# Kernel tuning notes

Measured on AMD Instinct MI355X. Metric: run time of the kernel, lower is better.

Reference implementation:

```python
import jax, jax.numpy as jnp
import numpy as np

N_NODES = 50000
N_EDGES = 800000
C_FEAT = 96
HID = 96
C_CONST = 0.005


def _psi(v):
    return jnp.sign(v) * jnp.log(jnp.abs(v) + 1.0)


def setup_inputs() -> dict:
    key = jax.random.key(0)
    ks = jax.random.split(key, 16)
    d_e_in = 2 * C_FEAT + 2
    d_h_in = 2 * C_FEAT
    def w(k, fan_in, fan_out):
        return jax.random.normal(k, (fan_in, fan_out), jnp.float32) * (1.0 / np.sqrt(fan_in))
    return {
        "x": jax.random.normal(ks[0], (N_NODES, 4), jnp.float32),
        "h": jax.random.normal(ks[1], (N_NODES, C_FEAT), jnp.float32),
        "edge_i": jax.random.randint(ks[2], (N_EDGES,), 0, N_NODES, jnp.int32),
        "edge_j": jax.random.randint(ks[3], (N_EDGES,), 0, N_NODES, jnp.int32),
        "We1": w(ks[4], d_e_in, HID), "be1": jnp.zeros((HID,), jnp.float32),
        "We2": w(ks[5], HID, HID), "be2": jnp.zeros((HID,), jnp.float32),
        "Wm": w(ks[6], HID, 1), "bm": jnp.zeros((1,), jnp.float32),
        "Wh1": w(ks[7], d_h_in, HID), "bh1": jnp.zeros((HID,), jnp.float32),
        "Wh2": w(ks[8], HID, C_FEAT), "bh2": jnp.zeros((C_FEAT,), jnp.float32),
        "Wx1": w(ks[9], HID, HID), "bx1": jnp.zeros((HID,), jnp.float32),
        "Wx2": w(ks[10], HID, 1),  # bias-free last phi_x layer
    }


def reference(x, h, edge_i, edge_j, We1, be1, We2, be2, Wm, bm,
              Wh1, bh1, Wh2, bh2, Wx1, bx1, Wx2):
    n = x.shape[0]
    x_i = x[edge_i]            # (K,4)
    x_j = x[edge_j]            # (K,4)
    # Minkowski invariants: 2*t-component - full Euclidean sum == (+,-,-,-)
    d2 = jnp.square(x_i - x_j)
    norms = 2.0 * d2[..., 0] - jnp.sum(d2, axis=-1)
    z = x_i * x_j
    prods = 2.0 * z[..., 0] - jnp.sum(z, axis=-1)
    norms = _psi(norms)[:, None]   # (K,1)
    prods = _psi(prods)[:, None]   # (K,1)

    e_in = jnp.concatenate([h[edge_i], h[edge_j], norms, prods], axis=-1)  # (K,2C+2)
    m = jax.nn.relu(jax.nn.relu(e_in @ We1 + be1) @ We2 + be2)             # (K,HID)
    w_gate = jax.nn.sigmoid(m @ Wm + bm)                                   # (K,1)

    wm = jax.ops.segment_sum(w_gate * m, edge_i, num_segments=n)          # (N,HID)
    dh = jax.nn.relu(jnp.concatenate([h, wm], axis=-1) @ Wh1 + bh1) @ Wh2 + bh2
    h_out = h + dh

    phi_x = jax.nn.relu(m @ Wx1 + bx1) @ Wx2                              # (K,1)
    vals = phi_x * x_j                                                     # (K,4)
    s = jax.ops.segment_sum(vals, edge_i, num_segments=n)                 # (N,4)
    cnt = jax.ops.segment_sum(jnp.ones((vals.shape[0],), vals.dtype), edge_i, num_segments=n)
    mean = jnp.where(cnt[:, None] > 0, s / jnp.maximum(cnt[:, None], 1.0), 0.0)
    x_out = x + C_CONST * mean
    return (h_out, x_out)
```

## Files before the change

### kernel.cpp

```cpp
#include <hip/hip_runtime.h>
#include <math.h>

#define NN 50000
#define NE 800000
#define NB 196

typedef __attribute__((ext_vector_type(8))) short short8v;
typedef __attribute__((ext_vector_type(4))) float f32x4;

__device__ __forceinline__ int rfl(int v) { return __builtin_amdgcn_readfirstlane(v); }
__device__ __forceinline__ unsigned short f2bf(float f) {
  unsigned u = __float_as_uint(f);
  u += 0x7FFFu + ((u >> 16) & 1u);
  return (unsigned short)(u >> 16);
}
__device__ __forceinline__ unsigned pk2(float a, float b) {
  return (unsigned)f2bf(a) | ((unsigned)f2bf(b) << 16);
}
__device__ __forceinline__ float bflo(unsigned u) { return __uint_as_float(u << 16); }
__device__ __forceinline__ float bfhi(unsigned u) { return __uint_as_float(u & 0xFFFF0000u); }

__global__ void khist(const int* __restrict__ ei, int* __restrict__ cnt) {
  const int i = blockIdx.x * 256 + threadIdx.x;
  atomicAdd(&cnt[ei[i]], 1);
}

__global__ void kscanA(const int* __restrict__ cnt, int* __restrict__ pre,
                       int* __restrict__ bsum) {
  __shared__ int ps[256];
  const int b = blockIdx.x, t = threadIdx.x, idx = b * 256 + t;
  const int v = (idx < NN) ? cnt[idx] : 0;
  ps[t] = v;
  __syncthreads();
  for (int off = 1; off < 256; off <<= 1) {
    const int u = (t >= off) ? ps[t - off] : 0;
    __syncthreads();
    ps[t] += u;
    __syncthreads();
  }
  if (idx < NN) pre[idx] = ps[t] - v;
  if (t == 255) bsum[b] = ps[255];
}

__global__ void kscanB(const int* __restrict__ bsum, int* __restrict__ boff) {
  __shared__ int ps[256];
  const int t = threadIdx.x;
  const int v = (t < NB) ? bsum[t] : 0;
  ps[t] = v;
  __syncthreads();
  for (int off = 1; off < 256; off <<= 1) {
    const int u = (t >= off) ? ps[t - off] : 0;
    __syncthreads();
    ps[t] += u;
    __syncthreads();
  }
  if (t < NB) boff[t] = ps[t] - v;
}

__global__ void kscanC(const int* __restrict__ pre, const int* __restrict__ boff,
                       int* __restrict__ base, int* __restrict__ cursor) {
  const int b = blockIdx.x, t = threadIdx.x, idx = b * 256 + t;
  if (idx < NN) {
    const int v = pre[idx] + boff[b];
    base[idx] = v;
    cursor[idx] = v;
  }
  if (idx == 0) base[NN] = NE;
}

__global__ void kperm(const int* __restrict__ ei, const int* __restrict__ ej,
                      int* __restrict__ cursor,
                      int* __restrict__ eis, int* __restrict__ ejs) {
  const int i = blockIdx.x * 256 + threadIdx.x;
  const int vi = ei[i];
  const int pos = atomicAdd(&cursor[vi], 1);
  eis[pos] = vi;
  ejs[pos] = ej[i];
}

__global__ void kwprep(const float* __restrict__ We1, const float* __restrict__ We2,
                       const float* __restrict__ Wx1, const float* __restrict__ Wh1,
                       const float* __restrict__ Wh2,
                       unsigned short* __restrict__ We1p, unsigned short* __restrict__ We2p,
                       unsigned short* __restrict__ Wx1p, unsigned short* __restrict__ Wh1p,
                       unsigned short* __restrict__ Wh2p) {
  const int t = blockIdx.x * 256 + threadIdx.x;
  const int j = t & 7, lane = (t >> 3) & 63;
  const int kk = (lane >> 4) * 8 + j;
  const int nn = lane & 15;
  {
    const int tile = t >> 9, tk = tile / 12, tn = tile % 12;
    const int k = tk * 32 + kk, n2 = tn * 16 + nn;
    const float v = (n2 < 96) ? We1[k * 96 + n2] : We1[(96 + k) * 96 + (n2 - 96)];
    We1p[t] = f2bf(v);
  }
  {
    const int tile = t >> 9, tk = tile / 6, tn = tile % 6;
    const int k = tk * 32 + kk, n = tn * 16 + nn;
    Wh1p[t] = f2bf(Wh1[k * 96 + n]);
  }
  if (t < 9216) {
    const int tile = t >> 9, tk = tile / 6, tn = tile % 6;
    const int k = tk * 32 + kk, n = tn * 16 + nn;
    We2p[t] = f2bf(We2[k * 96 + n]);
    Wx1p[t] = f2bf(Wx1[k * 96 + n]);
    Wh2p[t] = f2bf(Wh2[k * 96 + n]);
  }
}

__global__ __launch_bounds__(256, 4) void k0_AB(const float* __restrict__ h,
                                                const unsigned short* __restrict__ We1p,
                                                unsigned short* __restrict__ Abf,
                                                unsigned short* __restrict__ Bbf) {
  __shared__ __align__(16) unsigned short hbT[64 * 104];
  __shared__ __align__(16) unsigned short outT[64 * 200];
  const int tid = threadIdx.x;
  const int nb = blockIdx.x * 64;
  {
    const int e = tid & 63, q = tid >> 6;
    const int node = nb + e;
    const int nc = node < NN ? node : NN - 1;
    const float* hr = h + (long)nc * 96 + q * 24;
    unsigned* dst = (unsigned*)hbT + e * 52 + q * 12;
    #pragma unroll
    for (int c = 0; c < 6; ++c) {
      const float4 v = *(const float4*)(hr + c * 4);
      dst[c * 2]     = pk2(v.x, v.y);
      dst[c * 2 + 1] = pk2(v.z, v.w);
    }
  }
  __syncthreads();
  const int l = tid & 63, w = tid >> 6, cg = l & 15, rg = l >> 4;
  {
    const short8v* Wp = (const short8v*)We1p;
    const unsigned short* ar = hbT + (w * 16 + cg) * 104;
    const short8v af0 = *(const short8v*)(ar + rg * 8);
    const short8v af1 = *(const short8v*)(ar + 32 + rg * 8);
    const short8v af2 = *(const short8v*)(ar + 64 + rg * 8);
    #pragma unroll
    for (int tn = 0; tn < 12; ++tn) {
      f32x4 acc = (f32x4){0.f, 0.f, 0.f, 0.f};
      acc = __builtin_amdgcn_mfma_f32_16x16x32_bf16(af0, Wp[(0 * 12 + tn) * 64 + l], acc, 0, 0, 0);
      acc = __builtin_amdgcn_mfma_f32_16x16x32_bf16(af1, Wp[(1 * 12 + tn) * 64 + l], acc, 0, 0, 0);
      acc = __builtin_amdgcn_mfma_f32_16x16x32_bf16(af2, Wp[(2 * 12 + tn) * 64 + l], acc, 0, 0, 0);
      #pragma unroll
      for (int r = 0; r < 4; ++r)
        outT[(w * 16 + rg * 4 + r) * 200 + tn * 16 + cg] = f2bf(acc[r]);
    }
  }
  __syncthreads();
  {
    const int e = tid & 63, q = tid >> 6;
    const int node = nb + e;
    if (node < NN) {
      const unsigned* src = (const unsigned*)outT + e * 100;
      if (q < 2) {
        uint4* dA = (uint4*)(Abf + (size_t)node * 96);
        #pragma unroll
        for (int i = 0; i < 6; ++i) dA[q * 6 + i] = *(const uint4*)(src + (q * 6 + i) * 4);
      } else {
        uint4* dB = (uint4*)(Bbf + (size_t)node * 96);
        #pragma unroll
        for (int i = 0; i < 6; ++i) dB[(q - 2) * 6 + i] = *(const uint4*)(src + 48 + ((q - 2) * 6 + i) * 4);
      }
    }
  }
}

__global__ __launch_bounds__(256, 8) void k1_edge(const float* __restrict__ x,
    const unsigned short* __restrict__ Abf, const unsigned short* __restrict__ Bbf,
    const int* __restrict__ eis, const int* __restrict__ ejs,
    const float* __restrict__ We1, const float* __restrict__ be1,
    const unsigned short* __restrict__ We2p, const float* __restrict__ be2,
    const float* __restrict__ Wm, const float* __restrict__ bm,
    const unsigned short* __restrict__ Wx1p, const float* __restrict__ bx1,
    const float* __restrict__ Wx2,
    float* __restrict__ wmo, float* __restrict__ svo) {
  __shared__ __align__(16) unsigned short actT[64 * 104];
  __shared__ float gl[64];
  __shared__ float phil[64];
  __shared__ float xjl[64 * 4];
  __shared__ int vseq[66];

  const int tid = threadIdx.x;
  const float bm0 = bm[0];
  const int tb = blockIdx.x * 64;

  {
    const int e2 = tid & 63, fb = (tid >> 6) * 24;
    const int vi = eis[tb + e2], vj = ejs[tb + e2];
    const float4 xi = *(const float4*)(x + (long)vi * 4);
    const float4 xj = *(const float4*)(x + (long)vj * 4);
    if (tid < 64) {
      vseq[1 + e2] = vi;
      xjl[e2 * 4 + 0] = xj.x; xjl[e2 * 4 + 1] = xj.y;
      xjl[e2 * 4 + 2] = xj.z; xjl[e2 * 4 + 3] = xj.w;
    }
    if (tid == 0) {
      vseq[0]  = (tb > 0) ? eis[tb - 1] : -1;
      vseq[65] = (tb + 64 < NE) ? eis[tb + 64] : -1;
    }
    const float d0 = xi.x - xj.x, d1 = xi.y - xj.y, d2 = xi.z - xj.z, d3 = xi.w - xj.w;
    const float nrm = d0 * d0 - d1 * d1 - d2 * d2 - d3 * d3;
    const float prd = xi.x * xj.x - xi.y * xj.y - xi.z * xj.z - xi.w * xj.w;
    const float pn = copysignf(logf(fabsf(nrm) + 1.f), nrm);
    const float pp = copysignf(logf(fabsf(prd) + 1.f), prd);
    const uint4* Ar = (const uint4*)(Abf + (size_t)vi * 96 + fb);
    const uint4* Br = (const uint4*)(Bbf + (size_t)vj * 96 + fb);
    const uint4 A0 = Ar[0], A1 = Ar[1], A2 = Ar[2];
    const uint4 B0 = Br[0], B1 = Br[1], B2 = Br[2];
    unsigned ua[12], ub[12];
    ua[0]=A0.x; ua[1]=A0.y; ua[2]=A0.z; ua[3]=A0.w; ua[4]=A1.x; ua[5]=A1.y;
    ua[6]=A1.z; ua[7]=A1.w; ua[8]=A2.x; ua[9]=A2.y; ua[10]=A2.z; ua[11]=A2.w;
    ub[0]=B0.x; ub[1]=B0.y; ub[2]=B0.z; ub[3]=B0.w; ub[4]=B1.x; ub[5]=B1.y;
    ub[6]=B1.z; ub[7]=B1.w; ub[8]=B2.x; ub[9]=B2.y; ub[10]=B2.z; ub[11]=B2.w;
    unsigned* arow = (unsigned*)actT + e2 * 52 + fb / 2;
    #pragma unroll
    for (int p = 0; p < 12; ++p) {
      const int f = fb + 2 * p;
      const float lo = fmaxf(bflo(ua[p]) + bflo(ub[p]) + pn * We1[192 * 96 + f] + pp * We1[193 * 96 + f] + be1[f], 0.f);
      const float hi = fmaxf(bfhi(ua[p]) + bfhi(ub[p]) + pn * We1[192 * 96 + f + 1] + pp * We1[193 * 96 + f + 1] + be1[f + 1], 0.f);
      arow[p] = pk2(lo, hi);
    }
  }
  __syncthreads();

  const int l = tid & 63, w = tid >> 6;
  const int cg = l & 15, rg = l >> 4;
  const short8v* Wp2 = (const short8v*)We2p;
  const short8v* Wpx = (const short8v*)Wx1p;

  {
    const unsigned short* ar = actT + (w * 16 + cg) * 104;
    const short8v af0 = *(const short8v*)(ar + rg * 8);
    const short8v af1 = *(const short8v*)(ar + 32 + rg * 8);
    const short8v af2 = *(const short8v*)(ar + 64 + rg * 8);
    f32x4 acc[6];
    #pragma unroll
    for (int tn = 0; tn < 6; ++tn) acc[tn] = (f32x4){0.f, 0.f, 0.f, 0.f};
    #pragma unroll
    for (int tn = 0; tn < 6; ++tn) {
      acc[tn] = __builtin_amdgcn_mfma_f32_16x16x32_bf16(af0, Wp2[(0 * 6 + tn) * 64 + l], acc[tn], 0, 0, 0);
      acc[tn] = __builtin_amdgcn_mfma_f32_16x16x32_bf16(af1, Wp2[(1 * 6 + tn) * 64 + l], acc[tn], 0, 0, 0);
      acc[tn] = __builtin_amdgcn_mfma_f32_16x16x32_bf16(af2, Wp2[(2 * 6 + tn) * 64 + l], acc[tn], 0, 0, 0);
    }
    float gp[4] = {0.f, 0.f, 0.f, 0.f};
    #pragma unroll
    for (int tn = 0; tn < 6; ++tn) {
      const int col = tn * 16 + cg;
      const float b = be2[col], wmw = Wm[col];
      #pragma unroll
      for (int r = 0; r < 4; ++r) {
        const float v = fmaxf(acc[tn][r] + b, 0.f);
        gp[r] = fmaf(v, wmw, gp[r]);
        actT[(w * 16 + rg * 4 + r) * 104 + col] = (short)f2bf(v);
      }
    }
    #pragma unroll
    for (int r = 0; r < 4; ++r) {
      float s = gp[r];
      s += __shfl_xor(s, 1); s += __shfl_xor(s, 2);
      s += __shfl_xor(s, 4); s += __shfl_xor(s, 8);
      if (cg == 0) gl[w * 16 + rg * 4 + r] = 1.f / (1.f + expf(-(s + bm0)));
    }
  }
  __syncthreads();

  {
    const unsigned short* mr = actT + (w * 16 + cg) * 104;
    const short8v mf0 = *(const short8v*)(mr + rg * 8);
    const short8v mf1 = *(const short8v*)(mr + 32 + rg * 8);
    const short8v mf2 = *(const short8v*)(mr + 64 + rg * 8);
    f32x4 acc[6];
    #pragma unroll
    for (int tn = 0; tn < 6; ++tn) acc[tn] = (f32x4){0.f, 0.f, 0.f, 0.f};
    #pragma unroll
    for (int tn = 0; tn < 6; ++tn) {
      acc[tn] = __builtin_amdgcn_mfma_f32_16x16x32_bf16(mf0, Wpx[(0 * 6 + tn) * 64 + l], acc[tn], 0, 0, 0);
      acc[tn] = __builtin_amdgcn_mfma_f32_16x16x32_bf16(mf1, Wpx[(1 * 6 + tn) * 64 + l], acc[tn], 0, 0, 0);
      acc[tn] = __builtin_amdgcn_mfma_f32_16x16x32_bf16(mf2, Wpx[(2 * 6 + tn) * 64 + l], acc[tn], 0, 0, 0);
    }
    float pp2[4] = {0.f, 0.f, 0.f, 0.f};
    #pragma unroll
    for (int tn = 0; tn < 6; ++tn) {
      const int col = tn * 16 + cg;
      const float b = bx1[col], wxw = Wx2[col];
      #pragma unroll
      for (int r = 0; r < 4; ++r)
        pp2[r] = fmaf(fmaxf(acc[tn][r] + b, 0.f), wxw, pp2[r]);
    }
    #pragma unroll
    for (int r = 0; r < 4; ++r) {
      float s = pp2[r];
      s += __shfl_xor(s, 1); s += __shfl_xor(s, 2);
      s += __shfl_xor(s, 4); s += __shfl_xor(s, 8);
      if (cg == 0) phil[w * 16 + rg * 4 + r] = s;
    }
  }
  __syncthreads();

  if (tid < 200) {
    const bool isx = tid >= 192;
    const int col  = isx ? ((tid - 192) & 3) : (tid < 96 ? tid : tid - 96);
    const int half = isx ? ((tid - 192) >> 2) : (tid < 96 ? 0 : 1);
    const int s_lo = half * 32, s_hi = s_lo + 32;
    float acc = 0.f;
    bool clean = (vseq[s_lo] != vseq[s_lo + 1]);
    for (int e = s_lo; e < s_hi; ++e) {
      float val;
      if (isx) val = phil[e] * xjl[e * 4 + col];
      else     val = gl[e] * __uint_as_float(((unsigned)actT[e * 104 + col]) << 16);
      acc += val;
      const bool gend = (vseq[e + 1] != vseq[e + 2]);
      const bool last = (e == s_hi - 1);
      if (gend || last) {
        const int node = vseq[e + 1];
        float* dst = isx ? (svo + (size_t)node * 4 + col)
                         : (wmo + (size_t)node * 96 + col);
        if (clean && gend) *dst = acc; else atomicAdd(dst, acc);
        acc = 0.f; clean = true;
        if (last) break;
      }
    }
  }
}

__global__ __launch_bounds__(256, 4) void k3ab(const float* __restrict__ h,
    const float* __restrict__ wmv,
    const unsigned short* __restrict__ Wh1p, const float* __restrict__ bh1,
    const unsigned short* __restrict__ Wh2p, const float* __restrict__ bh2,
    const float* __restrict__ x, const float* __restrict__ svm,
    const int* __restrict__ basep,
    float* __restrict__ hout, float* __restrict__ xout) {
  __shared__ __align__(16) unsigned short inT[64 * 200];
  __shared__ __align__(16) unsigned short tmpT[64 * 104];
  const int tid = threadIdx.x;
  const int nb = blockIdx.x * 64;
  {
    const int e = tid & 63, q = tid >> 6;
    const int node = nb + e;
    const int nc = node < NN ? node : NN - 1;
    const float* hr = h + (long)nc * 96 + q * 24;
    const float* wr = wmv + (long)nc * 96 + q * 24;
    unsigned* dh = (unsigned*)inT + e * 100 + q * 12;
    unsigned* dw = (unsigned*)inT + e * 100 + 48 + q * 12;
    #pragma unroll
    for (int c = 0; c < 6; ++c) {
      const float4 v = *(const float4*)(hr + c * 4);
      dh[c * 2]     = pk2(v.x, v.y);
      dh[c * 2 + 1] = pk2(v.z, v.w);
      const float4 u = *(const float4*)(wr + c * 4);
      dw[c * 2]     = pk2(u.x, u.y);
      dw[c * 2 + 1] = pk2(u.z, u.w);
    }
  }
  __syncthreads();
  const int l = tid & 63, w = tid >> 6, cg = l & 15, rg = l >> 4;
  {
    const unsigned short* ar = inT + (w * 16 + cg) * 200;
    short8v af[6];
    #pragma unroll
    for (int tk = 0; tk < 6; ++tk) af[tk] = *(const short8v*)(ar + tk * 32 + rg * 8);
    const short8v* Wp = (const short8v*)Wh1p;
    #pragma unroll
    for (int tn = 0; tn < 6; ++tn) {
      f32x4 acc = (f32x4){0.f, 0.f, 0.f, 0.f};
      #pragma unroll
      for (int tk = 0; tk < 6; ++tk)
        acc = __builtin_amdgcn_mfma_f32_16x16x32_bf16(af[tk], Wp[(tk * 6 + tn) * 64 + l], acc, 0, 0, 0);
      const int col = tn * 16 + cg;
      const float b = bh1[col];
      #pragma unroll
      for (int r = 0; r < 4; ++r)
        tmpT[(w * 16 + rg * 4 + r) * 104 + col] = f2bf(fmaxf(acc[r] + b, 0.f));
    }
  }
  __syncthreads();
  {
    float* oT = (float*)inT;
    const unsigned short* mr = tmpT + (w * 16 + cg) * 104;
    const short8v mf0 = *(const short8v*)(mr + rg * 8);
    const short8v mf1 = *(const short8v*)(mr + 32 + rg * 8);
    const short8v mf2 = *(const short8v*)(mr + 64 + rg * 8);
    const short8v* Wp = (const short8v*)Wh2p;
    #pragma unroll
    for (int tn = 0; tn < 6; ++tn) {
      f32x4 acc = (f32x4){0.f, 0.f, 0.f, 0.f};
      acc = __builtin_amdgcn_mfma_f32_16x16x32_bf16(mf0, Wp[(0 * 6 + tn) * 64 + l], acc, 0, 0, 0);
      acc = __builtin_amdgcn_mfma_f32_16x16x32_bf16(mf1, Wp[(1 * 6 + tn) * 64 + l], acc, 0, 0, 0);
      acc = __builtin_amdgcn_mfma_f32_16x16x32_bf16(mf2, Wp[(2 * 6 + tn) * 64 + l], acc, 0, 0, 0);
      const int col = tn * 16 + cg;
      const float b = bh2[col];
      #pragma unroll
      for (int r = 0; r < 4; ++r)
        oT[(w * 16 + rg * 4 + r) * 100 + col] = acc[r] + b;
    }
  }
  __syncthreads();
  {
    const int e = tid & 63, q = tid >> 6;
    const int node = nb + e;
    if (node < NN) {
      const float* src = (const float*)inT + e * 100 + q * 24;
      const float* hr = h + (size_t)node * 96 + q * 24;
      float* dst = hout + (size_t)node * 96 + q * 24;
      #pragma unroll
      for (int c = 0; c < 6; ++c) {
        const float4 s = *(const float4*)(src + c * 4);
        const float4 hv = *(const float4*)(hr + c * 4);
        *(float4*)(dst + c * 4) = make_float4(hv.x + s.x, hv.y + s.y, hv.z + s.z, hv.w + s.w);
      }
    }
  }
  if (tid < 64) {
    const int node = nb + tid;
    if (node < NN) {
      const int cnt = basep[node + 1] - basep[node];
      const float inv = cnt > 0 ? 1.f / (float)cnt : 0.f;
      const float4 s4 = *(const float4*)(svm + (long)node * 4);
      const float4 xv = *(const float4*)(x + (long)node * 4);
      *(float4*)(xout + (long)node * 4) =
          make_float4(xv.x + 0.005f * s4.x * inv, xv.y + 0.005f * s4.y * inv,
                      xv.z + 0.005f * s4.z * inv, xv.w + 0.005f * s4.w * inv);
    }
  }
}

extern "C" void kernel_launch(void* const* d_in, const int* in_sizes, int n_in,
                              void* d_out, int out_size, void* d_ws, size_t ws_size,
                              hipStream_t stream) {
  const float* x   = (const float*)d_in[0];
  const float* h   = (const float*)d_in[1];
  const int*   ei  = (const int*)d_in[2];
  const int*   ej  = (const int*)d_in[3];
  const float* We1 = (const float*)d_in[4];
  const float* be1 = (const float*)d_in[5];
  const float* We2 = (const float*)d_in[6];
  const float* be2 = (const float*)d_in[7];
  const float* Wm  = (const float*)d_in[8];
  const float* bm  = (const float*)d_in[9];
  const float* Wh1 = (const float*)d_in[10];
  const float* bh1 = (const float*)d_in[11];
  const float* Wh2 = (const float*)d_in[12];
  const float* bh2 = (const float*)d_in[13];
  const float* Wx1 = (const float*)d_in[14];
  const float* bx1 = (const float*)d_in[15];
  const float* Wx2 = (const float*)d_in[16];

  char* w = (char*)d_ws;
  unsigned short* Abf  = (unsigned short*)w;
  unsigned short* Bbf  = (unsigned short*)(w + 9600000);
  float* WMv  = (float*)(w + 19200000);
  float* SvM  = (float*)(w + 38400000);
  int*   cnt  = (int*)(w + 39200000);
  int*   base = (int*)(w + 39400000);
  int*   curs = (int*)(w + 39600064);
  unsigned short* We2p = (unsigned short*)(w + 39800064);
  unsigned short* Wx1p = (unsigned short*)(w + 39818496);
  unsigned short* We1p = (unsigned short*)(w + 39836928);
  unsigned short* Wh1p = (unsigned short*)(w + 39873792);
  unsigned short* Wh2p = (unsigned short*)(w + 39910656);
  int*   eis  = (int*)(w + 39929088);
  int*   ejs  = (int*)(w + 43129088);
  int*   pre  = (int*)(w + 46329088);
  int*   bsum = (int*)(w + 46529088);
  int*   boff = (int*)(w + 46529872);

  float* hout = (float*)d_out;
  float* xout = hout + 4800000;

  hipMemsetAsync(cnt, 0, NN * sizeof(int), stream);
  hipMemsetAsync(WMv, 0, (size_t)(4800000 + 200000) * sizeof(float), stream);
  khist<<<NE / 256, 256, 0, stream>>>(ei, cnt);
  kscanA<<<NB, 256, 0, stream>>>(cnt, pre, bsum);
  kscanB<<<1, 256, 0, stream>>>(bsum, boff);
  kscanC<<<NB, 256, 0, stream>>>(pre, boff, base, curs);
  kperm<<<NE / 256, 256, 0, stream>>>(ei, ej, curs, eis, ejs);
  kwprep<<<72, 256, 0, stream>>>(We1, We2, Wx1, Wh1, Wh2, We1p, We2p, Wx1p, Wh1p, Wh2p);
  k0_AB<<<782, 256, 0, stream>>>(h, We1p, Abf, Bbf);
  k1_edge<<<NE / 64, 256, 0, stream>>>(x, Abf, Bbf, eis, ejs, We1, be1, We2p, be2,
                                       Wm, bm, Wx1p, bx1, Wx2, WMv, SvM);
  k3ab<<<782, 256, 0, stream>>>(h, WMv, Wh1p, bh1, Wh2p, bh2, x, SvM, base, hout, xout);
}
```

Measured before the change: 316.3 us.

## Process 128 edges per block with two MFMA row tiles sharing weight loads

The edge kernel now handles 128 edges per 256-thread block instead of 64. Each wave computes two 16-row tiles so every loaded weight fragment feeds two MFMAs, and one barrier between the two GEMMs is dropped because each wave only touches its own rows. Segment boundaries are precomputed once into ballot bitmasks, and the reduction is split across threads in two passes. In exchange it uses more registers and LDS (launch bounds drop to 5 blocks per CU) and produces half as many blocks, which may lower occupancy and latency hiding for the gathers.

```diff
diff --git a/kernel.cpp b/kernel.cpp
--- a/kernel.cpp
+++ b/kernel.cpp
@@ -4,6 +4,7 @@
 #define NN 50000
 #define NE 800000
 #define NB 196
+#define TE 128
 
 typedef __attribute__((ext_vector_type(8))) short short8v;
 typedef __attribute__((ext_vector_type(4))) float f32x4;
@@ -167,7 +168,7 @@
   }
 }
 
-__global__ __launch_bounds__(256, 8) void k1_edge(const float* __restrict__ x,
+__global__ __launch_bounds__(256, 5) void k1_edge(const float* __restrict__ x,
     const unsigned short* __restrict__ Abf, const unsigned short* __restrict__ Bbf,
     const int* __restrict__ eis, const int* __restrict__ ejs,
     const float* __restrict__ We1, const float* __restrict__ be1,
@@ -176,29 +177,30 @@
     const unsigned short* __restrict__ Wx1p, const float* __restrict__ bx1,
     const float* __restrict__ Wx2,
     float* __restrict__ wmo, float* __restrict__ svo) {
-  __shared__ __align__(16) unsigned short actT[64 * 104];
-  __shared__ float gl[64];
-  __shared__ float phil[64];
-  __shared__ float xjl[64 * 4];
-  __shared__ int vseq[66];
+  __shared__ __align__(16) unsigned short actT[TE * 104];
+  __shared__ float gl[TE];
+  __shared__ float phil[TE];
+  __shared__ __align__(16) float xjl[TE * 4];
+  __shared__ int vseq[TE + 2];
+  __shared__ unsigned long long bmask[2];
 
   const int tid = threadIdx.x;
   const float bm0 = bm[0];
-  const int tb = blockIdx.x * 64;
-
-  {
-    const int e2 = tid & 63, fb = (tid >> 6) * 24;
+  const int tb = blockIdx.x * TE;
+
+  {
+    const int e2 = tid & 127, hf = tid >> 7;
+    const int fb = hf * 48;
     const int vi = eis[tb + e2], vj = ejs[tb + e2];
     const float4 xi = *(const float4*)(x + (long)vi * 4);
     const float4 xj = *(const float4*)(x + (long)vj * 4);
-    if (tid < 64) {
+    if (hf == 0) {
       vseq[1 + e2] = vi;
-      xjl[e2 * 4 + 0] = xj.x; xjl[e2 * 4 + 1] = xj.y;
-      xjl[e2 * 4 + 2] = xj.z; xjl[e2 * 4 + 3] = xj.w;
+      *(float4*)(xjl + e2 * 4) = xj;
     }
     if (tid == 0) {
-      vseq[0]  = (tb > 0) ? eis[tb - 1] : -1;
-      vseq[65] = (tb + 64 < NE) ? eis[tb + 64] : -1;
+      vseq[0] = (tb > 0) ? eis[tb - 1] : -1;
+      vseq[TE + 1] = (tb + TE < NE) ? eis[tb + TE] : -1;
     }
     const float d0 = xi.x - xj.x, d1 = xi.y - xj.y, d2 = xi.z - xj.z, d3 = xi.w - xj.w;
     const float nrm = d0 * d0 - d1 * d1 - d2 * d2 - d3 * d3;
@@ -207,119 +209,165 @@
     const float pp = copysignf(logf(fabsf(prd) + 1.f), prd);
     const uint4* Ar = (const uint4*)(Abf + (size_t)vi * 96 + fb);
     const uint4* Br = (const uint4*)(Bbf + (size_t)vj * 96 + fb);
-    const uint4 A0 = Ar[0], A1 = Ar[1], A2 = Ar[2];
-    const uint4 B0 = Br[0], B1 = Br[1], B2 = Br[2];
-    unsigned ua[12], ub[12];
-    ua[0]=A0.x; ua[1]=A0.y; ua[2]=A0.z; ua[3]=A0.w; ua[4]=A1.x; ua[5]=A1.y;
-    ua[6]=A1.z; ua[7]=A1.w; ua[8]=A2.x; ua[9]=A2.y; ua[10]=A2.z; ua[11]=A2.w;
-    ub[0]=B0.x; ub[1]=B0.y; ub[2]=B0.z; ub[3]=B0.w; ub[4]=B1.x; ub[5]=B1.y;
-    ub[6]=B1.z; ub[7]=B1.w; ub[8]=B2.x; ub[9]=B2.y; ub[10]=B2.z; ub[11]=B2.w;
-    unsigned* arow = (unsigned*)actT + e2 * 52 + fb / 2;
-    #pragma unroll
-    for (int p = 0; p < 12; ++p) {
-      const int f = fb + 2 * p;
-      const float lo = fmaxf(bflo(ua[p]) + bflo(ub[p]) + pn * We1[192 * 96 + f] + pp * We1[193 * 96 + f] + be1[f], 0.f);
-      const float hi = fmaxf(bfhi(ua[p]) + bfhi(ub[p]) + pn * We1[192 * 96 + f + 1] + pp * We1[193 * 96 + f + 1] + be1[f + 1], 0.f);
-      arow[p] = pk2(lo, hi);
-    }
-  }
-  __syncthreads();
+    const float* wA = We1 + 192 * 96 + fb;
+    const float* wB = We1 + 193 * 96 + fb;
+    const float* bE = be1 + fb;
+    unsigned* arow = (unsigned*)actT + e2 * 52 + hf * 24;
+    #pragma unroll
+    for (int c = 0; c < 6; ++c) {
+      const uint4 A4 = Ar[c], B4 = Br[c];
+      const unsigned au[4] = {A4.x, A4.y, A4.z, A4.w};
+      const unsigned bu[4] = {B4.x, B4.y, B4.z, B4.w};
+      #pragma unroll
+      for (int k2 = 0; k2 < 4; ++k2) {
+        const int f = c * 8 + k2 * 2;
+        const float lo = fmaxf(bflo(au[k2]) + bflo(bu[k2]) + pn * wA[f] + pp * wB[f] + bE[f], 0.f);
+        const float hi = fmaxf(bfhi(au[k2]) + bfhi(bu[k2]) + pn * wA[f + 1] + pp * wB[f + 1] + bE[f + 1], 0.f);
+        arow[c * 4 + k2] = pk2(lo, hi);
+      }
+    }
+  }
+  __syncthreads();
+
+  if (tid < TE) {
+    const int pred = (vseq[1 + tid] != vseq[2 + tid]) ? 1 : 0;
+    const unsigned long long mk = __ballot(pred);
+    if ((tid & 63) == 0) bmask[tid >> 6] = mk;
+  }
 
   const int l = tid & 63, w = tid >> 6;
   const int cg = l & 15, rg = l >> 4;
+  const int r0 = w * 32;
   const short8v* Wp2 = (const short8v*)We2p;
   const short8v* Wpx = (const short8v*)Wx1p;
 
   {
-    const unsigned short* ar = actT + (w * 16 + cg) * 104;
-    const short8v af0 = *(const short8v*)(ar + rg * 8);
-    const short8v af1 = *(const short8v*)(ar + 32 + rg * 8);
-    const short8v af2 = *(const short8v*)(ar + 64 + rg * 8);
-    f32x4 acc[6];
-    #pragma unroll
-    for (int tn = 0; tn < 6; ++tn) acc[tn] = (f32x4){0.f, 0.f, 0.f, 0.f};
-    #pragma unroll
-    for (int tn = 0; tn < 6; ++tn) {
-      acc[tn] = __builtin_amdgcn_mfma_f32_16x16x32_bf16(af0, Wp2[(0 * 6 + tn) * 64 + l], acc[tn], 0, 0, 0);
-      acc[tn] = __builtin_amdgcn_mfma_f32_16x16x32_bf16(af1, Wp2[(1 * 6 + tn) * 64 + l], acc[tn], 0, 0, 0);
-      acc[tn] = __builtin_amdgcn_mfma_f32_16x16x32_bf16(af2, Wp2[(2 * 6 + tn) * 64 + l], acc[tn], 0, 0, 0);
-    }
-    float gp[4] = {0.f, 0.f, 0.f, 0.f};
-    #pragma unroll
-    for (int tn = 0; tn < 6; ++tn) {
-      const int col = tn * 16 + cg;
-      const float b = be2[col], wmw = Wm[col];
+    short8v af[2][3];
+    #pragma unroll
+    for (int rt = 0; rt < 2; ++rt)
+      #pragma unroll
+      for (int tk = 0; tk < 3; ++tk)
+        af[rt][tk] = *(const short8v*)(actT + (r0 + rt * 16 + cg) * 104 + tk * 32 + rg * 8);
+    f32x4 acc[2][6];
+    #pragma unroll
+    for (int rt = 0; rt < 2; ++rt)
+      #pragma unroll
+      for (int tn = 0; tn < 6; ++tn) acc[rt][tn] = (f32x4){0.f, 0.f, 0.f, 0.f};
+    #pragma unroll
+    for (int tk = 0; tk < 3; ++tk)
+      #pragma unroll
+      for (int tn = 0; tn < 6; ++tn) {
+        const short8v bf = Wp2[(tk * 6 + tn) * 64 + l];
+        acc[0][tn] = __builtin_amdgcn_mfma_f32_16x16x32_bf16(af[0][tk], bf, acc[0][tn], 0, 0, 0);
+        acc[1][tn] = __builtin_amdgcn_mfma_f32_16x16x32_bf16(af[1][tk], bf, acc[1][tn], 0, 0, 0);
+      }
+    #pragma unroll
+    for (int rt = 0; rt < 2; ++rt) {
+      float gp[4] = {0.f, 0.f, 0.f, 0.f};
+      #pragma unroll
+      for (int tn = 0; tn < 6; ++tn) {
+        const int col = tn * 16 + cg;
+        const float b = be2[col], wmw = Wm[col];
+        #pragma unroll
+        for (int r = 0; r < 4; ++r) {
+          const float v = fmaxf(acc[rt][tn][r] + b, 0.f);
+          gp[r] = fmaf(v, wmw, gp[r]);
+          actT[(r0 + rt * 16 + rg * 4 + r) * 104 + col] = (unsigned short)f2bf(v);
+        }
+      }
       #pragma unroll
       for (int r = 0; r < 4; ++r) {
-        const float v = fmaxf(acc[tn][r] + b, 0.f);
-        gp[r] = fmaf(v, wmw, gp[r]);
-        actT[(w * 16 + rg * 4 + r) * 104 + col] = (short)f2bf(v);
-      }
-    }
-    #pragma unroll
-    for (int r = 0; r < 4; ++r) {
-      float s = gp[r];
-      s += __shfl_xor(s, 1); s += __shfl_xor(s, 2);
-      s += __shfl_xor(s, 4); s += __shfl_xor(s, 8);
-      if (cg == 0) gl[w * 16 + rg * 4 + r] = 1.f / (1.f + expf(-(s + bm0)));
-    }
-  }
-  __syncthreads();
-
-  {
-    const unsigned short* mr = actT + (w * 16 + cg) * 104;
-    const short8v mf0 = *(const short8v*)(mr + rg * 8);
-    const short8v mf1 = *(const short8v*)(mr + 32 + rg * 8);
-    const short8v mf2 = *(const short8v*)(mr + 64 + rg * 8);
-    f32x4 acc[6];
-    #pragma unroll
-    for (int tn = 0; tn < 6; ++tn) acc[tn] = (f32x4){0.f, 0.f, 0.f, 0.f};
-    #pragma unroll
-    for (int tn = 0; tn < 6; ++tn) {
-      acc[tn] = __builtin_amdgcn_mfma_f32_16x16x32_bf16(mf0, Wpx[(0 * 6 + tn) * 64 + l], acc[tn], 0, 0, 0);
-      acc[tn] = __builtin_amdgcn_mfma_f32_16x16x32_bf16(mf1, Wpx[(1 * 6 + tn) * 64 + l], acc[tn], 0, 0, 0);
-      acc[tn] = __builtin_amdgcn_mfma_f32_16x16x32_bf16(mf2, Wpx[(2 * 6 + tn) * 64 + l], acc[tn], 0, 0, 0);
-    }
-    float pp2[4] = {0.f, 0.f, 0.f, 0.f};
-    #pragma unroll
-    for (int tn = 0; tn < 6; ++tn) {
-      const int col = tn * 16 + cg;
-      const float b = bx1[col], wxw = Wx2[col];
-      #pragma unroll
-      for (int r = 0; r < 4; ++r)
-        pp2[r] = fmaf(fmaxf(acc[tn][r] + b, 0.f), wxw, pp2[r]);
-    }
-    #pragma unroll
-    for (int r = 0; r < 4; ++r) {
-      float s = pp2[r];
-      s += __shfl_xor(s, 1); s += __shfl_xor(s, 2);
-      s += __shfl_xor(s, 4); s += __shfl_xor(s, 8);
-      if (cg == 0) phil[w * 16 + rg * 4 + r] = s;
-    }
-  }
-  __syncthreads();
-
-  if (tid < 200) {
-    const bool isx = tid >= 192;
-    const int col  = isx ? ((tid - 192) & 3) : (tid < 96 ? tid : tid - 96);
-    const int half = isx ? ((tid - 192) >> 2) : (tid < 96 ? 0 : 1);
-    const int s_lo = half * 32, s_hi = s_lo + 32;
-    float acc = 0.f;
-    bool clean = (vseq[s_lo] != vseq[s_lo + 1]);
-    for (int e = s_lo; e < s_hi; ++e) {
-      float val;
-      if (isx) val = phil[e] * xjl[e * 4 + col];
-      else     val = gl[e] * __uint_as_float(((unsigned)actT[e * 104 + col]) << 16);
-      acc += val;
-      const bool gend = (vseq[e + 1] != vseq[e + 2]);
-      const bool last = (e == s_hi - 1);
-      if (gend || last) {
+        float s = gp[r];
+        s += __shfl_xor(s, 1); s += __shfl_xor(s, 2);
+        s += __shfl_xor(s, 4); s += __shfl_xor(s, 8);
+        if (cg == 0) gl[r0 + rt * 16 + rg * 4 + r] = 1.f / (1.f + expf(-(s + bm0)));
+      }
+    }
+  }
+
+
+  {
+    short8v af[2][3];
+    #pragma unroll
+    for (int rt = 0; rt < 2; ++rt)
+      #pragma unroll
+      for (int tk = 0; tk < 3; ++tk)
+        af[rt][tk] = *(const short8v*)(actT + (r0 + rt * 16 + cg) * 104 + tk * 32 + rg * 8);
+    f32x4 acc[2][6];
+    #pragma unroll
+    for (int rt = 0; rt < 2; ++rt)
+      #pragma unroll
+      for (int tn = 0; tn < 6; ++tn) acc[rt][tn] = (f32x4){0.f, 0.f, 0.f, 0.f};
+    #pragma unroll
+    for (int tk = 0; tk < 3; ++tk)
+      #pragma unroll
+      for (int tn = 0; tn < 6; ++tn) {
+        const short8v bf = Wpx[(tk * 6 + tn) * 64 + l];
+        acc[0][tn] = __builtin_amdgcn_mfma_f32_16x16x32_bf16(af[0][tk], bf, acc[0][tn], 0, 0, 0);
+        acc[1][tn] = __builtin_amdgcn_mfma_f32_16x16x32_bf16(af[1][tk], bf, acc[1][tn], 0, 0, 0);
+      }
+    #pragma unroll
+    for (int rt = 0; rt < 2; ++rt) {
+      float pp2[4] = {0.f, 0.f, 0.f, 0.f};
+      #pragma unroll
+      for (int tn = 0; tn < 6; ++tn) {
+        const int col = tn * 16 + cg;
+        const float b = bx1[col], wxw = Wx2[col];
+        #pragma unroll
+        for (int r = 0; r < 4; ++r)
+          pp2[r] = fmaf(fmaxf(acc[rt][tn][r] + b, 0.f), wxw, pp2[r]);
+      }
+      #pragma unroll
+      for (int r = 0; r < 4; ++r) {
+        float s = pp2[r];
+        s += __shfl_xor(s, 1); s += __shfl_xor(s, 2);
+        s += __shfl_xor(s, 4); s += __shfl_xor(s, 8);
+        if (cg == 0) phil[r0 + rt * 16 + rg * 4 + r] = s;
+      }
+    }
+  }
+  __syncthreads();
+
+  if (tid < 192) {
+    const int q0 = (tid >= 96) ? 1 : 0;
+    const int col = tid - 96 * q0;
+    #pragma unroll
+    for (int pass = 0; pass < 2; ++pass) {
+      const int q = q0 + 2 * pass;
+      const int s_lo = q * 32;
+      const unsigned long long mk = bmask[s_lo >> 6];
+      float acc2 = 0.f;
+      bool clean = (q == 0) ? (vseq[0] != vseq[1])
+                            : (((bmask[(s_lo - 1) >> 6] >> ((s_lo - 1) & 63)) & 1ull) != 0);
+      for (int i = 0; i < 32; ++i) {
+        const int e = s_lo + i;
+        acc2 = fmaf(gl[e], __uint_as_float(((unsigned)actT[e * 104 + col]) << 16), acc2);
+        const bool gend = ((mk >> (e & 63)) & 1ull) != 0;
+        if (gend || i == 31) {
+          const int node = vseq[e + 1];
+          float* dst = wmo + (size_t)node * 96 + col;
+          if (clean && gend) *dst = acc2; else atomicAdd(dst, acc2);
+          acc2 = 0.f; clean = true;
+        }
+      }
+    }
+  } else if (tid < 224) {
+    const int t2 = tid - 192;
+    const int comp = t2 & 3, q8 = t2 >> 2;
+    const int s_lo = q8 * 16;
+    const unsigned long long mk = bmask[s_lo >> 6];
+    float acc2 = 0.f;
+    bool clean = (q8 == 0) ? (vseq[0] != vseq[1])
+                           : (((bmask[(s_lo - 1) >> 6] >> ((s_lo - 1) & 63)) & 1ull) != 0);
+    for (int i = 0; i < 16; ++i) {
+      const int e = s_lo + i;
+      acc2 = fmaf(phil[e], xjl[e * 4 + comp], acc2);
+      const bool gend = ((mk >> (e & 63)) & 1ull) != 0;
+      if (gend || i == 15) {
         const int node = vseq[e + 1];
-        float* dst = isx ? (svo + (size_t)node * 4 + col)
-                         : (wmo + (size_t)node * 96 + col);
-        if (clean && gend) *dst = acc; else atomicAdd(dst, acc);
-        acc = 0.f; clean = true;
-        if (last) break;
+        float* dst = svo + (size_t)node * 4 + comp;
+        if (clean && gend) *dst = acc2; else atomicAdd(dst, acc2);
+        acc2 = 0.f; clean = true;
       }
     }
   }
@@ -478,7 +526,7 @@
   kperm<<<NE / 256, 256, 0, stream>>>(ei, ej, curs, eis, ejs);
   kwprep<<<72, 256, 0, stream>>>(We1, We2, Wx1, Wh1, Wh2, We1p, We2p, Wx1p, Wh1p, Wh2p);
   k0_AB<<<782, 256, 0, stream>>>(h, We1p, Abf, Bbf);
-  k1_edge<<<NE / 64, 256, 0, stream>>>(x, Abf, Bbf, eis, ejs, We1, be1, We2p, be2,
+  k1_edge<<<NE / TE, 256, 0, stream>>>(x, Abf, Bbf, eis, ejs, We1, be1, We2p, be2,
                                        Wm, bm, Wx1p, bx1, Wx2, WMv, SvM);
   k3ab<<<782, 256, 0, stream>>>(h, WMv, Wh1p, bh1, Wh2p, bh2, x, SvM, base, hout, xout);
 }
```

Result: no change. 312.7 us (-1.1%).
